# Optimization experiments

Hardware: AMD Instinct MI355X
Metric: run time of the kernel (lower is better)

The kernel has to match this reference:

```python
import jax, jax.numpy as jnp
import numpy as np

B, C_TEXT, C, T, S, K = 4, 192, 768, 2048, 1024, 12


def setup_inputs() -> dict:
    key = jax.random.key(0)
    ks = jax.random.split(key, 6)
    return {
        "y": jax.random.normal(ks[0], (B, C, T), jnp.float32),
        "y_mask": jnp.ones((B, T), jnp.float32),
        "text": jax.random.normal(ks[1], (B, C_TEXT, S), jnp.float32),
        "text_mask": jnp.ones((B, S), jnp.float32),
        "ge": jax.random.normal(ks[2], (B, C, 1), jnp.float32),
        "W": jax.random.normal(ks[3], (K, C, C_TEXT), jnp.float32) * 0.05,
        "b": jax.random.normal(ks[4], (K, C), jnp.float32) * 0.01,
        "scale": jnp.ones((K,), jnp.float32),
    }


def reference(y, y_mask, text, text_mask, ge, W, b, scale):
    # 12 parallel 1x1-conv projections, batched: [K,B,C,S]
    tp = jnp.einsum('koc,bcs->kbos', W, text) + b[:, None, :, None]
    tp = tp * scale[:, None, None, None]
    tp = tp * text_mask[None, :, None, :]          # mask text positions
    # cross-attention scores for all 12 heads: [K,B,T,S]
    attn = jnp.einsum('bct,kbcs->kbts', y, tp)
    attn_mask = y_mask[:, :, None] * text_mask[:, None, :]   # [B,T,S]
    attn = attn * attn_mask[None] / jnp.sqrt(jnp.float32(C))
    attn = jax.nn.softmax(attn, axis=-1)
    # per-head context summed over heads: [B,C_text,T]... note context uses raw text (192 ch)
    context = jnp.einsum('kbts,bcs->bct', attn, text)        # sums over k and s
    # original adds 12 contexts of shape [B,192,T]; broadcast-add against y [B,768,T]
    # mirrors torch broadcasting only if channel dims match -> pad context to C via tile? No:
    # torch einsum 'bts,bcs->bct' with text [B,192,S] yields [B,192,T]; y is [B,768,T].
    # Faithful to the code as written, the add relies on matching channels, so we
    # project context into C by zero-padding is NOT in source; instead the source
    # implies context channels == y channels. We follow source semantics: contexts
    # are computed against raw text; to keep shapes consistent we broadcast via tiling
    context = jnp.tile(context, (1, C // C_TEXT, 1))
    out = y + context + ge
    return out
```

## Files before the change

kernel.cpp:

```cpp
#include <hip/hip_runtime.h>
#include <hip/hip_bf16.h>

#define BB 4
#define CC 768
#define CT 192
#define TT 2048
#define SS 1024
#define KK 12

typedef __attribute__((ext_vector_type(8))) short bfrag8;
typedef __attribute__((ext_vector_type(4))) float f32x4;


__device__ inline unsigned pk2(float a, float b) {
    __hip_bfloat162 h2;
    h2.x = __float2bfloat16(a);
    h2.y = __float2bfloat16(b);
    return *reinterpret_cast<unsigned*>(&h2);
}
__device__ inline float unpk_lo(unsigned u) { return __uint_as_float(u << 16); }
__device__ inline float unpk_hi(unsigned u) {
    return __uint_as_float(u & 0xffff0000u);
}

__global__ __launch_bounds__(256) void k_pack_all(
    const float* __restrict__ text, const float* __restrict__ W,
    const float* __restrict__ y, __hip_bfloat16* __restrict__ textS,
    __hip_bfloat16* __restrict__ textC, __hip_bfloat16* __restrict__ WP,
    __hip_bfloat16* __restrict__ yP) {
    __shared__ float tile[32][64];
    const int blk = blockIdx.x;
    const int tid = threadIdx.x;

    if (blk < 32) {
        const int b = blk >> 3;
        const float* tb = text + (size_t)b * CT * SS;
        const int base = tid + (blk & 7) * 256;
        for (int e = base; e < 64 * 6 * 512; e += 2048) {
            int jj = e & 7, l = (e >> 3) & 63, cc = (e >> 9) % 6, st = e / 3072;
            int ct = cc * 32 + ((l >> 4) << 3) + jj;
            int s = st * 16 + (l & 15);
            textS[(size_t)b * 196608 + e] =
                __float2bfloat16(tb[(size_t)ct * SS + s]);
        }
        for (int e = base; e < 12 * 32 * 512; e += 2048) {
            int jj = e & 7, l = (e >> 3) & 63, scg = (e >> 9) & 31,
                ctt = e / 16384;
            int ct = ctt * 16 + (l & 15);
            int s = scg * 32 + ((l >> 4) << 3) + jj;
            textC[(size_t)b * 196608 + e] =
                __float2bfloat16(tb[(size_t)ct * SS + s]);
        }
    } else if (blk < 128) {
        const int k = (blk - 32) >> 3;
        const float* wk = W + (size_t)k * CC * CT;
        const int base = tid + ((blk - 32) & 7) * 256;
        for (int e = base; e < 12 * 24 * 512; e += 2048) {
            int j = e & 7, l = (e >> 3) & 63, oc = (e >> 9) % 24, nt = e / 12288;
            int ct = nt * 16 + (l & 15);
            int o = oc * 32 + ((l >> 4) << 3) + j;
            WP[(size_t)k * 147456 + e] =
                __float2bfloat16(wk[(size_t)o * CT + ct]);
        }
    } else {
        const int idx = blk - 128;
        const int b = idx >> 5;
        const int tq = idx & 31;
        const int t0 = tq * 64;
        const float* yb_ = y + (size_t)b * CC * TT;
        const int w = tid >> 6, l = tid & 63;
        const int l15 = l & 15, lg = l >> 4;
        const int row0 = tid >> 4;
        const int c4 = tid & 15;

        for (int oc = 0; oc < 24; ++oc) {
#pragma unroll
            for (int h = 0; h < 2; ++h) {
                const int row = row0 + h * 16;
                const float4 v = *reinterpret_cast<const float4*>(
                    yb_ + (size_t)(oc * 32 + row) * TT + t0 + c4 * 4);
                *reinterpret_cast<float4*>(&tile[row][c4 * 4]) = v;
            }
            __syncthreads();
            union {
                bfrag8 v8;
                short u[8];
            } A;
#pragma unroll
            for (int j = 0; j < 8; ++j)
                A.u[j] = (short)__bfloat16_as_ushort(
                    __float2bfloat16(tile[lg * 8 + j][w * 16 + l15]));
            __hip_bfloat16* dst =
                yP + (((size_t)(b * 128 + tq * 4 + w) * 24 + oc) * 512) +
                (size_t)l * 8;
            *reinterpret_cast<bfrag8*>(dst) = A.v8;
            __syncthreads();
        }
    }
}

__global__ __launch_bounds__(256, 2) void k_yw_mfma(
    const __hip_bfloat16* __restrict__ yP, const __hip_bfloat16* __restrict__ WP,
    __hip_bfloat16* __restrict__ ywA) {
    const int i = blockIdx.x;
    const int x = i & 7, j = i >> 3;
    const int b = x & 3;
    const int k = j >> 4;
    const int tx = (j & 15) | ((x >> 2) << 4);
    const int kb = k * BB + b;

    const int tid = threadIdx.x;
    const int w = tid >> 6, l = tid & 63;
    const int l15 = l & 15, lg = l >> 4;
    const int ttg0 = tx * 4;
    const int nt0 = 3 * w;

    __shared__ float ot[4][16][197];

    const short* ypb = reinterpret_cast<const short*>(yP) +
                       (((size_t)b * 128 + ttg0) * 24) * 512 + (size_t)l * 8;
    const short* wp = reinterpret_cast<const short*>(WP) +
                      (size_t)k * 147456 + (size_t)l * 8;

    f32x4 acc[3][4];
#pragma unroll
    for (int n = 0; n < 3; ++n)
#pragma unroll
        for (int tg = 0; tg < 4; ++tg) acc[n][tg] = (f32x4){0.f, 0.f, 0.f, 0.f};

    for (int oc = 0; oc < 24; ++oc) {
        bfrag8 af[4];
#pragma unroll
        for (int tg = 0; tg < 4; ++tg)
            af[tg] =
                *reinterpret_cast<const bfrag8*>(ypb + (tg * 24 + oc) * 512);
#pragma unroll
        for (int n = 0; n < 3; ++n) {
            bfrag8 bf = *reinterpret_cast<const bfrag8*>(
                wp + ((nt0 + n) * 24 + oc) * 512);
#pragma unroll
            for (int tg = 0; tg < 4; ++tg)
                acc[n][tg] = __builtin_amdgcn_mfma_f32_16x16x32_bf16(
                    af[tg], bf, acc[n][tg], 0, 0, 0);
        }
    }

#pragma unroll
    for (int n = 0; n < 3; ++n) {
        const int ct = (w * 3 + n) * 16 + l15;
#pragma unroll
        for (int tg = 0; tg < 4; ++tg)
#pragma unroll
            for (int r = 0; r < 4; ++r) ot[tg][lg * 4 + r][ct] = acc[n][tg][r];
    }
    __syncthreads();

    const size_t obase = ((size_t)kb * 128 + ttg0 + w) * 3072;
#pragma unroll
    for (int cc = 0; cc < 6; ++cc) {
        union {
            bfrag8 v8;
            short u[8];
        } A;
#pragma unroll
        for (int j2 = 0; j2 < 8; ++j2)
            A.u[j2] = (short)__bfloat16_as_ushort(
                __float2bfloat16(ot[w][l15][cc * 32 + lg * 8 + j2]));
        *reinterpret_cast<bfrag8*>(
            reinterpret_cast<short*>(ywA) + obase + cc * 512 + (size_t)l * 8) =
            A.v8;
    }
}

__global__ __launch_bounds__(256) void k_yb2(const float* __restrict__ y,
                                             const float* __restrict__ bias,
                                             float* __restrict__ yb) {
    const int b = blockIdx.y;
    const int t0 = blockIdx.x * 64;
    const int tid = threadIdx.x;
    const int tl = tid & 63, g = tid >> 6;

    __shared__ float bs[KK][CC];
    __shared__ float pb[4][64][KK];
    for (int i = tid; i < KK * CC; i += 256) bs[i / CC][i % CC] = bias[i];
    __syncthreads();

    float p[KK];
#pragma unroll
    for (int k = 0; k < KK; ++k) p[k] = 0.f;
    const float* yb_ = y + (size_t)b * CC * TT + t0 + tl;
    for (int o = g * 192; o < g * 192 + 192; ++o) {
        float v = yb_[(size_t)o * TT];
#pragma unroll
        for (int k = 0; k < KK; ++k) p[k] += v * bs[k][o];
    }
#pragma unroll
    for (int k = 0; k < KK; ++k) pb[g][tl][k] = p[k];
    __syncthreads();
    for (int i = tid; i < 64 * KK; i += 256) {
        int tt = i / KK, k = i % KK;
        float s = pb[0][tt][k] + pb[1][tt][k] + pb[2][tt][k] + pb[3][tt][k];
        yb[((size_t)k * BB + b) * TT + t0 + tt] = s;
    }
}

__global__ __launch_bounds__(512) void k_attn_fused(
    const float* __restrict__ ymask, const float* __restrict__ tmask,
    const float* __restrict__ scale, const __hip_bfloat16* __restrict__ ywA,
    const float* __restrict__ ybws, const __hip_bfloat16* __restrict__ textS,
    const __hip_bfloat16* __restrict__ textC, const float* __restrict__ y,
    const float* __restrict__ ge, float* __restrict__ out) {
    const int i = blockIdx.x;
    const int x = i & 7;
    const int b = x & 3;
    const int tt = (i >> 3) + ((x >> 2) << 6);
    const int t0 = tt * 16;
    const int tid = threadIdx.x;
    const int w = tid >> 6;
    const int l = tid & 63;
    const int l15 = l & 15, lg = l >> 4;
    const int ws0 = w * 128;

    __shared__ float lds_acc[8][8][64][4];
    __shared__ uint2 exp_buf[2][8][8][64];
    __shared__ __align__(16) short af_s[2][6][64][8];
    __shared__ float yb_s[KK][16];
    __shared__ float sc_s[KK];
    __shared__ __align__(16) float lred[2][2][16][8];

    if (tid < 192)
        yb_s[tid >> 4][tid & 15] =
            ybws[(size_t)((tid >> 4) * BB + b) * TT + t0 + (tid & 15)];
    if (tid < KK) sc_s[tid] = scale[tid];
    const f32x4 zero4 = (f32x4){0.f, 0.f, 0.f, 0.f};
#pragma unroll
    for (int st = 0; st < 8; ++st)
        *reinterpret_cast<f32x4*>(&lds_acc[w][st][l][0]) = zero4;

    float tm2r[8];
#pragma unroll
    for (int st = 0; st < 8; ++st) {
        float m = tmask[b * SS + ws0 + st * 16 + l15];
        tm2r[st] = m * m;
    }
    float ymr[4];
#pragma unroll
    for (int r = 0; r < 4; ++r) ymr[r] = ymask[b * TT + t0 + lg * 4 + r];
    const float invs_l2e = 0.03608439182435161f * 1.4426950408889634f;

    const short* ywAs = reinterpret_cast<const short*>(ywA);
    const short* tS = reinterpret_cast<const short*>(textS);
    const short* tSw = tS + (((size_t)b * 64 + w * 8) * 6) * 512 + (size_t)l * 8;
    const size_t headStride = (size_t)BB * 128 * 3072;

    for (int kp = 0; kp < 6; ++kp) {
        const size_t ab0_l0 =
            (((size_t)(2 * kp * BB + b) * 128 + tt) * 6) * 512;
        for (int u = tid; u < 768; u += 512) {
            const int p = u / 384;
            const int rem = u - p * 384;
            const int cc2 = rem >> 6;
            const int l2 = rem & 63;
            bfrag8 v = *reinterpret_cast<const bfrag8*>(
                ywAs + ab0_l0 + (size_t)p * headStride + cc2 * 512 + l2 * 8);
            *reinterpret_cast<bfrag8*>(&af_s[p][cc2][l2][0]) = v;
        }
        __syncthreads();

        float cfr[2][4], ybk[2][4];
#pragma unroll
        for (int p = 0; p < 2; ++p) {
            const int k = 2 * kp + p;
            const float sk = sc_s[k] * invs_l2e;
#pragma unroll
            for (int r = 0; r < 4; ++r) {
                const float cf = sk * ymr[r];
                cfr[p][r] = cf;
                ybk[p][r] = yb_s[k][lg * 4 + r] * cf;
            }
        }

        bfrag8 bfc[6];
#pragma unroll
        for (int cc = 0; cc < 6; ++cc)
            bfc[cc] = *reinterpret_cast<const bfrag8*>(tSw + cc * 512);

        float lrow[2][4] = {{0.f, 0.f, 0.f, 0.f}, {0.f, 0.f, 0.f, 0.f}};
#pragma unroll
        for (int st = 0; st < 8; ++st) {
            f32x4 av0 = zero4, av1 = zero4;
            __builtin_amdgcn_s_setprio(1);
#pragma unroll
            for (int cc = 0; cc < 6; ++cc) {
                bfrag8 a0 =
                    *reinterpret_cast<const bfrag8*>(&af_s[0][cc][l][0]);
                bfrag8 a1 =
                    *reinterpret_cast<const bfrag8*>(&af_s[1][cc][l][0]);
                av0 = __builtin_amdgcn_mfma_f32_16x16x32_bf16(a0, bfc[cc],
                                                              av0, 0, 0, 0);
                av1 = __builtin_amdgcn_mfma_f32_16x16x32_bf16(a1, bfc[cc],
                                                              av1, 0, 0, 0);
            }
            __builtin_amdgcn_s_setprio(0);
            if (st < 7) {
#pragma unroll
                for (int cc = 0; cc < 6; ++cc)
                    bfc[cc] = *reinterpret_cast<const bfrag8*>(
                        tSw + ((st + 1) * 6 + cc) * 512);
            }
#pragma unroll
            for (int r = 0; r < 4; ++r) {
                float e0 = exp2f((av0[r] * cfr[0][r] + ybk[0][r]) * tm2r[st]);
                float e1 = exp2f((av1[r] * cfr[1][r] + ybk[1][r]) * tm2r[st]);
                av0[r] = e0;
                av1[r] = e1;
                lrow[0][r] += e0;
                lrow[1][r] += e1;
            }
            exp_buf[0][w][st][l] =
                make_uint2(pk2(av0[0], av0[1]), pk2(av0[2], av0[3]));
            exp_buf[1][w][st][l] =
                make_uint2(pk2(av1[0], av1[1]), pk2(av1[2], av1[3]));
        }

#pragma unroll
        for (int d = 1; d < 16; d <<= 1)
#pragma unroll
            for (int p = 0; p < 2; ++p)
#pragma unroll
                for (int r = 0; r < 4; ++r)
                    lrow[p][r] += __shfl_xor(lrow[p][r], d);
        if (l15 == 0) {
#pragma unroll
            for (int p = 0; p < 2; ++p)
#pragma unroll
                for (int r = 0; r < 4; ++r)
                    lred[kp & 1][p][lg * 4 + r][w] = lrow[p][r];
        }
        __syncthreads();
        float rl[2][4];
#pragma unroll
        for (int p = 0; p < 2; ++p)
#pragma unroll
            for (int r = 0; r < 4; ++r) {
                const float4 v0 = *reinterpret_cast<const float4*>(
                    &lred[kp & 1][p][lg * 4 + r][0]);
                const float4 v1 = *reinterpret_cast<const float4*>(
                    &lred[kp & 1][p][lg * 4 + r][4]);
                rl[p][r] = 1.0f / (v0.x + v0.y + v0.z + v0.w + v1.x + v1.y +
                                   v1.z + v1.w);
            }
#pragma unroll
        for (int st = 0; st < 8; ++st) {
            const uint2 e0 = exp_buf[0][w][st][l];
            const uint2 e1 = exp_buf[1][w][st][l];
            f32x4 cur = *reinterpret_cast<f32x4*>(&lds_acc[w][st][l][0]);
            cur[0] += unpk_lo(e0.x) * rl[0][0] + unpk_lo(e1.x) * rl[1][0];
            cur[1] += unpk_hi(e0.x) * rl[0][1] + unpk_hi(e1.x) * rl[1][1];
            cur[2] += unpk_lo(e0.y) * rl[0][2] + unpk_lo(e1.y) * rl[1][2];
            cur[3] += unpk_hi(e0.y) * rl[0][3] + unpk_hi(e1.y) * rl[1][3];
            *reinterpret_cast<f32x4*>(&lds_acc[w][st][l][0]) = cur;
        }
    }
    __builtin_amdgcn_s_waitcnt(0);

    const short* tC = reinterpret_cast<const short*>(textC);
    f32x4 cacc[12];
#pragma unroll
    for (int c = 0; c < 12; ++c) cacc[c] = (f32x4){0.f, 0.f, 0.f, 0.f};

#pragma unroll
    for (int sc = 0; sc < 4; ++sc) {
        const int scg = w * 4 + sc;
        union {
            bfrag8 v8;
            unsigned u[4];
        } A;
#pragma unroll
        for (int jp = 0; jp < 4; ++jp) {
            const int s0 = scg * 32 + lg * 8 + jp * 2;
            const int reg0 = s0 >> 7, st0 = (s0 >> 4) & 7;
            const int lo0 = (s0 & 15) | ((l15 >> 2) << 4);
            const int s1 = s0 + 1;
            const int lo1 = (s1 & 15) | ((l15 >> 2) << 4);
            const int ro = l15 & 3;
            float a = lds_acc[reg0][st0][lo0][ro];
            float bb2 = lds_acc[s1 >> 7][(s1 >> 4) & 7][lo1][ro];
            A.u[jp] = pk2(a, bb2);
        }
#pragma unroll
        for (int ctt = 0; ctt < 12; ++ctt) {
            bfrag8 bf = *reinterpret_cast<const bfrag8*>(
                tC + (((size_t)b * 12 + ctt) * 32 + scg) * 512 + (size_t)l * 8);
            cacc[ctt] = __builtin_amdgcn_mfma_f32_16x16x32_bf16(
                A.v8, bf, cacc[ctt], 0, 0, 0);
        }
    }
    __syncthreads();

    float(*part)[16][192] =
        reinterpret_cast<float(*)[16][192]>(&lds_acc[0][0][0][0]);
    if (w < 4) {
#pragma unroll
        for (int ctt = 0; ctt < 12; ++ctt)
#pragma unroll
            for (int r = 0; r < 4; ++r)
                part[w][lg * 4 + r][ctt * 16 + l15] = cacc[ctt][r];
    }
    __syncthreads();
    if (w >= 4) {
#pragma unroll
        for (int ctt = 0; ctt < 12; ++ctt)
#pragma unroll
            for (int r = 0; r < 4; ++r)
                part[w - 4][lg * 4 + r][ctt * 16 + l15] += cacc[ctt][r];
    }
    __syncthreads();

    const float* yb_ = y + (size_t)b * CC * TT;
    float* ob = out + (size_t)b * CC * TT;
    const float* geb = ge + b * CC;
    for (int c = tid; c < CC; c += 512) {
        const float gev = geb[c];
        const int cm = c % CT;
        const float4* ysrc =
            reinterpret_cast<const float4*>(yb_ + (size_t)c * TT + t0);
        float4* od = reinterpret_cast<float4*>(ob + (size_t)c * TT + t0);
#pragma unroll
        for (int i4 = 0; i4 < 4; ++i4) {
            float4 v = ysrc[i4];
            const int row = i4 * 4;
            v.x += part[0][row + 0][cm] + part[1][row + 0][cm] +
                   part[2][row + 0][cm] + part[3][row + 0][cm] + gev;
            v.y += part[0][row + 1][cm] + part[1][row + 1][cm] +
                   part[2][row + 1][cm] + part[3][row + 1][cm] + gev;
            v.z += part[0][row + 2][cm] + part[1][row + 2][cm] +
                   part[2][row + 2][cm] + part[3][row + 2][cm] + gev;
            v.w += part[0][row + 3][cm] + part[1][row + 3][cm] +
                   part[2][row + 3][cm] + part[3][row + 3][cm] + gev;
            od[i4] = v;
        }
    }
}

extern "C" void kernel_launch(void* const* d_in, const int* in_sizes, int n_in,
                              void* d_out, int out_size, void* d_ws,
                              size_t ws_size, hipStream_t stream) {
    const float* y      = (const float*)d_in[0];
    const float* ymask  = (const float*)d_in[1];
    const float* text   = (const float*)d_in[2];
    const float* tmask  = (const float*)d_in[3];
    const float* ge     = (const float*)d_in[4];
    const float* W      = (const float*)d_in[5];
    const float* bias   = (const float*)d_in[6];
    const float* scale  = (const float*)d_in[7];
    float* out = (float*)d_out;

    char* ws = (char*)d_ws;
    __hip_bfloat16* ywA   = (__hip_bfloat16*)ws;
    float*          ybws  = (float*)(ws + 37748736);
    __hip_bfloat16* textS = (__hip_bfloat16*)(ws + 38141952);
    __hip_bfloat16* textC = (__hip_bfloat16*)(ws + 39714816);
    __hip_bfloat16* yP    = (__hip_bfloat16*)(ws + 58064896);
    __hip_bfloat16* WP    = (__hip_bfloat16*)(ws + 70647808);

    k_pack_all<<<256, 256, 0, stream>>>(text, W, y, textS, textC, WP, yP);
    k_yb2<<<dim3(TT / 64, BB), 256, 0, stream>>>(y, bias, ybws);
    k_yw_mfma<<<1536, 256, 0, stream>>>(yP, WP, ywA);
    k_attn_fused<<<512, 512, 0, stream>>>(ymask, tmask, scale, ywA, ybws,
                                          textS, textC, y, ge, out);
}
```

Before: 221.1 us.

## Fuse bias-projection into pack kernel and double-buffer MFMA operand loads

Merges the separate y·bias reduction kernel into the packing kernel as extra blocks, which removes one launch and lets that work run alongside packing. The y·W MFMA kernel now register-double-buffers its A/B fragments so the next oc step's loads overlap the current MFMAs. The attention kernel double-buffers the per-head-pair ywA LDS tile and prefetches the next pair during the exp phase, dropping a barrier per iteration. In exchange it uses more registers and LDS, and the larger 48KB shared buffer in the pack kernel may reduce its occupancy.

Result: slower. 238.2 us (+7.8%).

```diff
diff --git a/kernel.cpp b/kernel.cpp
--- a/kernel.cpp
+++ b/kernel.cpp
@@ -25,10 +25,11 @@
 
 __global__ __launch_bounds__(256) void k_pack_all(
     const float* __restrict__ text, const float* __restrict__ W,
-    const float* __restrict__ y, __hip_bfloat16* __restrict__ textS,
-    __hip_bfloat16* __restrict__ textC, __hip_bfloat16* __restrict__ WP,
-    __hip_bfloat16* __restrict__ yP) {
-    __shared__ float tile[32][64];
+    const float* __restrict__ y, const float* __restrict__ bias,
+    __hip_bfloat16* __restrict__ textS, __hip_bfloat16* __restrict__ textC,
+    __hip_bfloat16* __restrict__ WP, __hip_bfloat16* __restrict__ yP,
+    float* __restrict__ ybws) {
+    __shared__ __align__(16) char pk_lds[49152];
     const int blk = blockIdx.x;
     const int tid = threadIdx.x;
 
@@ -62,7 +63,8 @@
             WP[(size_t)k * 147456 + e] =
                 __float2bfloat16(wk[(size_t)o * CT + ct]);
         }
-    } else {
+    } else if (blk < 256) {
+        float(*tile)[64] = reinterpret_cast<float(*)[64]>(pk_lds);
         const int idx = blk - 128;
         const int b = idx >> 5;
         const int tq = idx & 31;
@@ -96,6 +98,37 @@
             *reinterpret_cast<bfrag8*>(dst) = A.v8;
             __syncthreads();
         }
+    } else {
+        float(*bs)[CC] = reinterpret_cast<float(*)[CC]>(pk_lds);
+        float(*pb)[32][KK] =
+            reinterpret_cast<float(*)[32][KK]>(pk_lds + 36864);
+        const int idx = blk - 256;
+        const int b = idx >> 6;
+        const int t0 = (idx & 63) * 32;
+        const int tl = tid & 31, g = tid >> 5;
+
+        for (int i = tid; i < KK * CC; i += 256) bs[i / CC][i % CC] = bias[i];
+        __syncthreads();
+
+        float p[KK];
+#pragma unroll
+        for (int k = 0; k < KK; ++k) p[k] = 0.f;
+        const float* yb_ = y + (size_t)b * CC * TT + t0 + tl;
+        for (int o = g * 96; o < g * 96 + 96; ++o) {
+            float v = yb_[(size_t)o * TT];
+#pragma unroll
+            for (int k = 0; k < KK; ++k) p[k] += v * bs[k][o];
+        }
+#pragma unroll
+        for (int k = 0; k < KK; ++k) pb[g][tl][k] = p[k];
+        __syncthreads();
+        for (int i = tid; i < 32 * KK; i += 256) {
+            int t = i / KK, k = i % KK;
+            float s = 0.f;
+#pragma unroll
+            for (int gg = 0; gg < 8; ++gg) s += pb[gg][t][k];
+            ybws[((size_t)k * BB + b) * TT + t0 + t] = s;
+        }
     }
 }
 
@@ -128,21 +161,33 @@
 #pragma unroll
         for (int tg = 0; tg < 4; ++tg) acc[n][tg] = (f32x4){0.f, 0.f, 0.f, 0.f};
 
+    bfrag8 af[2][4], bf[2][3];
+#pragma unroll
+    for (int tg = 0; tg < 4; ++tg)
+        af[0][tg] = *reinterpret_cast<const bfrag8*>(ypb + (tg * 24) * 512);
+#pragma unroll
+    for (int n = 0; n < 3; ++n)
+        bf[0][n] = *reinterpret_cast<const bfrag8*>(wp + ((nt0 + n) * 24) * 512);
+
+#pragma unroll
     for (int oc = 0; oc < 24; ++oc) {
-        bfrag8 af[4];
-#pragma unroll
-        for (int tg = 0; tg < 4; ++tg)
-            af[tg] =
-                *reinterpret_cast<const bfrag8*>(ypb + (tg * 24 + oc) * 512);
-#pragma unroll
-        for (int n = 0; n < 3; ++n) {
-            bfrag8 bf = *reinterpret_cast<const bfrag8*>(
-                wp + ((nt0 + n) * 24 + oc) * 512);
+        const int cur = oc & 1, nxt = cur ^ 1;
+        if (oc < 23) {
+#pragma unroll
+            for (int tg = 0; tg < 4; ++tg)
+                af[nxt][tg] = *reinterpret_cast<const bfrag8*>(
+                    ypb + (tg * 24 + oc + 1) * 512);
+#pragma unroll
+            for (int n = 0; n < 3; ++n)
+                bf[nxt][n] = *reinterpret_cast<const bfrag8*>(
+                    wp + ((nt0 + n) * 24 + oc + 1) * 512);
+        }
+#pragma unroll
+        for (int n = 0; n < 3; ++n)
 #pragma unroll
             for (int tg = 0; tg < 4; ++tg)
                 acc[n][tg] = __builtin_amdgcn_mfma_f32_16x16x32_bf16(
-                    af[tg], bf, acc[n][tg], 0, 0, 0);
-        }
+                    af[cur][tg], bf[cur][n], acc[n][tg], 0, 0, 0);
     }
 
 #pragma unroll
@@ -169,38 +214,6 @@
         *reinterpret_cast<bfrag8*>(
             reinterpret_cast<short*>(ywA) + obase + cc * 512 + (size_t)l * 8) =
             A.v8;
-    }
-}
-
-__global__ __launch_bounds__(256) void k_yb2(const float* __restrict__ y,
-                                             const float* __restrict__ bias,
-                                             float* __restrict__ yb) {
-    const int b = blockIdx.y;
-    const int t0 = blockIdx.x * 64;
-    const int tid = threadIdx.x;
-    const int tl = tid & 63, g = tid >> 6;
-
-    __shared__ float bs[KK][CC];
-    __shared__ float pb[4][64][KK];
-    for (int i = tid; i < KK * CC; i += 256) bs[i / CC][i % CC] = bias[i];
-    __syncthreads();
-
-    float p[KK];
-#pragma unroll
-    for (int k = 0; k < KK; ++k) p[k] = 0.f;
-    const float* yb_ = y + (size_t)b * CC * TT + t0 + tl;
-    for (int o = g * 192; o < g * 192 + 192; ++o) {
-        float v = yb_[(size_t)o * TT];
-#pragma unroll
-        for (int k = 0; k < KK; ++k) p[k] += v * bs[k][o];
-    }
-#pragma unroll
-    for (int k = 0; k < KK; ++k) pb[g][tl][k] = p[k];
-    __syncthreads();
-    for (int i = tid; i < 64 * KK; i += 256) {
-        int tt = i / KK, k = i % KK;
-        float s = pb[0][tt][k] + pb[1][tt][k] + pb[2][tt][k] + pb[3][tt][k];
-        yb[((size_t)k * BB + b) * TT + t0 + tt] = s;
     }
 }
 
@@ -223,7 +236,7 @@
 
     __shared__ float lds_acc[8][8][64][4];
     __shared__ uint2 exp_buf[2][8][8][64];
-    __shared__ __align__(16) short af_s[2][6][64][8];
+    __shared__ __align__(16) short af_s[2][2][6][64][8];
     __shared__ float yb_s[KK][16];
     __shared__ float sc_s[KK];
     __shared__ __align__(16) float lred[2][2][16][8];
@@ -253,9 +266,8 @@
     const short* tSw = tS + (((size_t)b * 64 + w * 8) * 6) * 512 + (size_t)l * 8;
     const size_t headStride = (size_t)BB * 128 * 3072;
 
-    for (int kp = 0; kp < 6; ++kp) {
-        const size_t ab0_l0 =
-            (((size_t)(2 * kp * BB + b) * 128 + tt) * 6) * 512;
+    {
+        const size_t ab0_l0 = (((size_t)(0 * BB + b) * 128 + tt) * 6) * 512;
         for (int u = tid; u < 768; u += 512) {
             const int p = u / 384;
             const int rem = u - p * 384;
@@ -263,10 +275,13 @@
             const int l2 = rem & 63;
             bfrag8 v = *reinterpret_cast<const bfrag8*>(
                 ywAs + ab0_l0 + (size_t)p * headStride + cc2 * 512 + l2 * 8);
-            *reinterpret_cast<bfrag8*>(&af_s[p][cc2][l2][0]) = v;
-        }
-        __syncthreads();
-
+            *reinterpret_cast<bfrag8*>(&af_s[0][p][cc2][l2][0]) = v;
+        }
+    }
+    __syncthreads();
+
+    for (int kp = 0; kp < 6; ++kp) {
+        const int cb = kp & 1;
         float cfr[2][4], ybk[2][4];
 #pragma unroll
         for (int p = 0; p < 2; ++p) {
@@ -293,9 +308,9 @@
 #pragma unroll
             for (int cc = 0; cc < 6; ++cc) {
                 bfrag8 a0 =
-                    *reinterpret_cast<const bfrag8*>(&af_s[0][cc][l][0]);
+                    *reinterpret_cast<const bfrag8*>(&af_s[cb][0][cc][l][0]);
                 bfrag8 a1 =
-                    *reinterpret_cast<const bfrag8*>(&af_s[1][cc][l][0]);
+                    *reinterpret_cast<const bfrag8*>(&af_s[cb][1][cc][l][0]);
                 av0 = __builtin_amdgcn_mfma_f32_16x16x32_bf16(a0, bfc[cc],
                                                               av0, 0, 0, 0);
                 av1 = __builtin_amdgcn_mfma_f32_16x16x32_bf16(a1, bfc[cc],
@@ -323,6 +338,20 @@
                 make_uint2(pk2(av1[0], av1[1]), pk2(av1[2], av1[3]));
         }
 
+        if (kp < 5) {
+            const size_t abn =
+                (((size_t)(2 * (kp + 1) * BB + b) * 128 + tt) * 6) * 512;
+            for (int u = tid; u < 768; u += 512) {
+                const int p = u / 384;
+                const int rem = u - p * 384;
+                const int cc2 = rem >> 6;
+                const int l2 = rem & 63;
+                bfrag8 v = *reinterpret_cast<const bfrag8*>(
+                    ywAs + abn + (size_t)p * headStride + cc2 * 512 + l2 * 8);
+                *reinterpret_cast<bfrag8*>(&af_s[cb ^ 1][p][cc2][l2][0]) = v;
+            }
+        }
+
 #pragma unroll
         for (int d = 1; d < 16; d <<= 1)
 #pragma unroll
@@ -335,7 +364,7 @@
             for (int p = 0; p < 2; ++p)
 #pragma unroll
                 for (int r = 0; r < 4; ++r)
-                    lred[kp & 1][p][lg * 4 + r][w] = lrow[p][r];
+                    lred[cb][p][lg * 4 + r][w] = lrow[p][r];
         }
         __syncthreads();
         float rl[2][4];
@@ -344,9 +373,9 @@
 #pragma unroll
             for (int r = 0; r < 4; ++r) {
                 const float4 v0 = *reinterpret_cast<const float4*>(
-                    &lred[kp & 1][p][lg * 4 + r][0]);
+                    &lred[cb][p][lg * 4 + r][0]);
                 const float4 v1 = *reinterpret_cast<const float4*>(
-                    &lred[kp & 1][p][lg * 4 + r][4]);
+                    &lred[cb][p][lg * 4 + r][4]);
                 rl[p][r] = 1.0f / (v0.x + v0.y + v0.z + v0.w + v1.x + v1.y +
                                    v1.z + v1.w);
             }
@@ -464,8 +493,8 @@
     __hip_bfloat16* yP    = (__hip_bfloat16*)(ws + 58064896);
     __hip_bfloat16* WP    = (__hip_bfloat16*)(ws + 70647808);
 
-    k_pack_all<<<256, 256, 0, stream>>>(text, W, y, textS, textC, WP, yP);
-    k_yb2<<<dim3(TT / 64, BB), 256, 0, stream>>>(y, bias, ybws);
+    k_pack_all<<<512, 256, 0, stream>>>(text, W, y, bias, textS, textC, WP,
+                                        yP, ybws);
     k_yw_mfma<<<1536, 256, 0, stream>>>(yP, WP, ywA);
     k_attn_fused<<<512, 512, 0, stream>>>(ymask, tmask, scale, ywA, ybws,
                                           textS, textC, y, ge, out);
```
